# Performance work log

Hardware: AMD Instinct MI355X
Metric: run time of the kernel (lower is better)

Reference implementation:

```python
import jax, jax.numpy as jnp
import numpy as np

B, C_LOW, C_HIGH, KC, VC, H, W = 4, 512, 256, 64, 64, 64, 64


def setup_inputs() -> dict:
    key = jax.random.key(0)
    ks = jax.random.split(key, 6)
    x_low = jax.random.normal(ks[0], (B, C_LOW, H, W), dtype=jnp.float32)
    x_high = jax.random.normal(ks[1], (B, C_HIGH, H, W), dtype=jnp.float32)
    # 1x1 conv weights, fan-in scaled
    Wq = jax.random.normal(ks[2], (KC, C_HIGH), dtype=jnp.float32) / np.sqrt(C_HIGH)
    Wk = jax.random.normal(ks[3], (KC, C_LOW), dtype=jnp.float32) / np.sqrt(C_LOW)
    Wv = jax.random.normal(ks[4], (VC, C_LOW), dtype=jnp.float32) / np.sqrt(C_LOW)
    Wo = jax.random.normal(ks[5], (C_HIGH, VC), dtype=jnp.float32) / np.sqrt(VC)
    return {
        "x_low": x_low, "x_high": x_high,
        "Wq": Wq, "bq": jnp.zeros((KC,), jnp.float32),
        "Wk": Wk, "bk": jnp.zeros((KC,), jnp.float32),
        "Wv": Wv, "bv": jnp.zeros((VC,), jnp.float32),
        "Wo": Wo, "bo": jnp.zeros((C_HIGH,), jnp.float32),
    }


def reference(x_low, x_high, Wq, bq, Wk, bk, Wv, bv, Wo, bo):
    b, ch, h, w = x_high.shape
    n = h * w  # tokens per image
    # 1x1 convs == per-pixel linear maps; flatten spatial to tokens
    xh = x_high.reshape(b, ch, n)                # [B, C_high, N]
    xl = x_low.reshape(b, x_low.shape[1], n)     # [B, C_low,  N]
    q = jnp.einsum('kc,bcn->bnk', Wq, xh) + bq   # [B, N, KC]
    k = jnp.einsum('kc,bcn->bkn', Wk, xl) + bk[:, None]  # [B, KC, N]
    v = jnp.einsum('vc,bcn->bnv', Wv, xl) + bv   # [B, N, VC]
    sim = jnp.einsum('bnk,bkm->bnm', q, k)       # [B, N, N]
    attn = jax.nn.softmax(sim, axis=-1)
    ctx = jnp.einsum('bnm,bmv->bnv', attn, v)    # [B, N, VC]
    out = jnp.einsum('ov,bnv->bon', Wo, ctx) + bo[:, None]  # [B, C_high, N]
    return out.reshape(b, ch, h, w) + x_high
```

## Files before the change

### kernel.cpp

```cpp
#include <hip/hip_runtime.h>
#include <hip/hip_bf16.h>
#include <math.h>
#include <stdint.h>

#define B 4
#define CLOW 512
#define CHIGH 256
#define KC 64
#define VC 64
#define N 4096

typedef __attribute__((ext_vector_type(8))) short bf16x8;
typedef __attribute__((ext_vector_type(4))) short bf16x4;
typedef __attribute__((ext_vector_type(4))) float f32x4;

__device__ inline unsigned short f2bf(float f) {
    union { float f; uint32_t u; } v; v.f = f;
    uint32_t u = v.u;
    u += 0x7fff + ((u >> 16) & 1);
    return (unsigned short)(u >> 16);
}
__device__ inline float bf2f(unsigned short h) {
    union { uint32_t u; float f; } v; v.u = ((uint32_t)h) << 16;
    return v.f;
}
__device__ inline uint32_t packbf2(float a, float b) {
    union { __hip_bfloat16 h; unsigned short u; } ca, cb;
    ca.h = __float2bfloat16(a);
    cb.h = __float2bfloat16(b);
    return (uint32_t)ca.u | ((uint32_t)cb.u << 16);
}
__device__ inline void bfsplit(float x, short* hi, short* lo) {
    union { __hip_bfloat16 h; unsigned short u; } c, d;
    c.h = __float2bfloat16(x);
    d.h = __float2bfloat16(x - __bfloat162float(c.h));
    *hi = (short)c.u; *lo = (short)d.u;
}

#if __has_builtin(__builtin_amdgcn_exp2f)
#define EXP2(x) __builtin_amdgcn_exp2f(x)
#else
#define EXP2(x) exp2f(x)
#endif


#define CSTEP 64
__global__ __launch_bounds__(256) void proj_mfma(
    const float* __restrict__ xl, const float* __restrict__ xh,
    const float* __restrict__ Wq, const float* __restrict__ bq,
    const float* __restrict__ Wk, const float* __restrict__ bk,
    const float* __restrict__ Wv, const float* __restrict__ bv,
    unsigned short* __restrict__ Qt, unsigned short* __restrict__ Kt,
    unsigned short* __restrict__ Vt)
{
    const int proj = blockIdx.z;
    const int b    = blockIdx.y;
    const int bidx = blockIdx.x;
    const int n0   = bidx * 32;
    const int tid  = threadIdx.x;
    const int wv   = tid >> 6;
    const int lane = tid & 63;
    const int lo   = lane & 15;
    const int hi   = lane >> 4;
    const int hi8  = hi * 8;

    __shared__ unsigned short XtHi[32][72];
    __shared__ unsigned short XtLo[32][72];

    const int tS = tid & 3;
    const int t8 = tS * 8;
    const int cR = tid >> 2;

    const float* X; int C;
    if (proj == 0) { X = xh; C = CHIGH; } else { X = xl; C = CLOW; }

    float4 pf0, pf1;

    #define LOADX(C0)                                                            \
        {                                                                        \
            const float* src = X + ((size_t)b*C + (C0) + cR)*N + n0 + t8;        \
            pf0 = *(const float4*)src;                                           \
            pf1 = *(const float4*)(src + 4);                                     \
        }

    #define STAGE()                                                              \
        {                                                                        \
            const int colx = cR ^ (tS << 3);                                     \
            float vv[8] = {pf0.x, pf0.y, pf0.z, pf0.w,                           \
                           pf1.x, pf1.y, pf1.z, pf1.w};                          \
            _Pragma("unroll")                                                    \
            for (int i = 0; i < 8; ++i) {                                        \
                short h_, l_;                                                    \
                bfsplit(vv[i], &h_, &l_);                                        \
                XtHi[t8 + i][colx] = (unsigned short)h_;                         \
                XtLo[t8 + i][colx] = (unsigned short)l_;                         \
            }                                                                    \
        }

    #define WSPLITLD(WP, AH, AL)                                                 \
        {                                                                        \
            float4 w0 = *(const float4*)(WP);                                    \
            float4 w1 = *(const float4*)((WP) + 4);                              \
            float ww[8] = {w0.x,w0.y,w0.z,w0.w,w1.x,w1.y,w1.z,w1.w};             \
            _Pragma("unroll")                                                    \
            for (int i = 0; i < 8; ++i) {                                        \
                short h_, l_;                                                    \
                bfsplit(ww[i], &h_, &l_);                                        \
                AH[i] = h_; AL[i] = l_;                                          \
            }                                                                    \
        }

    const size_t kqFragOff = (size_t)((((wv*2 + (hi>>1)) & 3)*16 + lo)*8 + (hi&1)*4);

    if (proj == 0) {
        f32x4 acc[2];
        #pragma unroll
        for (int t = 0; t < 2; ++t)
            #pragma unroll
            for (int r = 0; r < 4; ++r) acc[t][r] = bq[wv*16 + hi*4 + r];

        LOADX(0)
        for (int c0 = 0; c0 < CHIGH; c0 += CSTEP) {
            STAGE()
            __syncthreads();
            if (c0 + CSTEP < CHIGH) LOADX(c0 + CSTEP)

            #pragma unroll
            for (int m = 0; m < 2; ++m) {
                bf16x8 ah, al;
                const float* wp = Wq + (size_t)(wv*16 + lo)*CHIGH + c0 + m*32 + hi8;
                WSPLITLD(wp, ah, al)
                #pragma unroll
                for (int tt = 0; tt < 2; ++tt) {
                    const int cx = (m*32 + hi8) ^ ((2*tt + (lo >> 3)) << 3);
                    bf16x8 xhv = *(const bf16x8*)&XtHi[tt*16 + lo][cx];
                    bf16x8 xlv = *(const bf16x8*)&XtLo[tt*16 + lo][cx];
                    acc[tt] = __builtin_amdgcn_mfma_f32_16x16x32_bf16(ah, xhv, acc[tt], 0, 0, 0);
                    acc[tt] = __builtin_amdgcn_mfma_f32_16x16x32_bf16(ah, xlv, acc[tt], 0, 0, 0);
                    acc[tt] = __builtin_amdgcn_mfma_f32_16x16x32_bf16(al, xhv, acc[tt], 0, 0, 0);
                }
            }
            __syncthreads();
        }
        const float qs = 1.4426950408889634f;
        #pragma unroll
        for (int t = 0; t < 2; ++t) {
            bf16x4 o;
            #pragma unroll
            for (int r = 0; r < 4; ++r) o[r] = (short)f2bf(acc[t][r] * qs);
            size_t base = (((size_t)b*256 + 2*bidx + t)*2 + (wv>>1))*512;
            *(bf16x4*)&Qt[base + kqFragOff] = o;
        }
    } else {
        f32x4 accK[2], accV[2];
        #pragma unroll
        for (int t = 0; t < 2; ++t)
            #pragma unroll
            for (int r = 0; r < 4; ++r) {
                accK[t][r] = bk[wv*16 + hi*4 + r];
                accV[t][r] = bv[wv*16 + hi*4 + r];
            }

        LOADX(0)
        for (int c0 = 0; c0 < CLOW; c0 += CSTEP) {
            STAGE()
            __syncthreads();
            if (c0 + CSTEP < CLOW) LOADX(c0 + CSTEP)

            #pragma unroll
            for (int m = 0; m < 2; ++m) {
                bf16x8 ahk, alk, ahv, alv;
                const float* wpk = Wk + (size_t)(wv*16 + lo)*CLOW + c0 + m*32 + hi8;
                const float* wpv = Wv + (size_t)(wv*16 + lo)*CLOW + c0 + m*32 + hi8;
                WSPLITLD(wpk, ahk, alk)
                WSPLITLD(wpv, ahv, alv)
                #pragma unroll
                for (int tt = 0; tt < 2; ++tt) {
                    const int cx = (m*32 + hi8) ^ ((2*tt + (lo >> 3)) << 3);
                    bf16x8 xhv = *(const bf16x8*)&XtHi[tt*16 + lo][cx];
                    bf16x8 xlv = *(const bf16x8*)&XtLo[tt*16 + lo][cx];
                    accK[tt] = __builtin_amdgcn_mfma_f32_16x16x32_bf16(ahk, xhv, accK[tt], 0, 0, 0);
                    accK[tt] = __builtin_amdgcn_mfma_f32_16x16x32_bf16(ahk, xlv, accK[tt], 0, 0, 0);
                    accK[tt] = __builtin_amdgcn_mfma_f32_16x16x32_bf16(alk, xhv, accK[tt], 0, 0, 0);
                    accV[tt] = __builtin_amdgcn_mfma_f32_16x16x32_bf16(ahv, xhv, accV[tt], 0, 0, 0);
                    accV[tt] = __builtin_amdgcn_mfma_f32_16x16x32_bf16(ahv, xlv, accV[tt], 0, 0, 0);
                    accV[tt] = __builtin_amdgcn_mfma_f32_16x16x32_bf16(alv, xhv, accV[tt], 0, 0, 0);
                }
            }
            __syncthreads();
        }

        #pragma unroll
        for (int t = 0; t < 2; ++t) {
            bf16x4 o;
            #pragma unroll
            for (int r = 0; r < 4; ++r) o[r] = (short)f2bf(accK[t][r]);
            size_t kbase = (((size_t)b*256 + 2*bidx + t)*2 + (wv>>1))*512;
            *(bf16x4*)&Kt[kbase + kqFragOff] = o;

            const int hi_f = t*2 + (lo >> 3);
            size_t vbase = ((size_t)b*128 + bidx)*2048 + (size_t)wv*512
                         + (size_t)hi_f*128 + (size_t)(lo & 7);
            #pragma unroll
            for (int r = 0; r < 4; ++r)
                Vt[vbase + (size_t)(hi*4 + r)*8] = f2bf(accV[t][r]);
        }
    }
    #undef LOADX
    #undef STAGE
    #undef WSPLITLD
}

#define WSPLIT 8
#define QT 4
__global__ __launch_bounds__(512) void attn(
    const unsigned short* __restrict__ Qt,
    const unsigned short* __restrict__ Kt,
    const unsigned short* __restrict__ Vt,
    float* __restrict__ ctx)
{
    const int bid = blockIdx.x;
    const int xcd = bid & 7;
    const int b   = xcd >> 1;
    const int q0  = ((bid >> 3) * 2 + (xcd & 1)) * 64;

    const int tid  = threadIdx.x;
    const int wv   = tid >> 6;
    const int lane = tid & 63;
    const int lo   = lane & 15;
    const int hi   = lane >> 4;

    __shared__ float Olds[WSPLIT][64][68];
    __shared__ float llds[WSPLIT][64];

    const unsigned short* Kb = Kt + (size_t)b*N*KC;
    const unsigned short* Vb = Vt + (size_t)b*VC*N;
    const unsigned short* Qb = Qt + (size_t)b*N*KC;

    bf16x8 qf[2][QT];
    #pragma unroll
    for (int qt = 0; qt < QT; ++qt) {
        #pragma unroll
        for (int kt = 0; kt < 2; ++kt)
            qf[kt][qt] = *(const bf16x8*)&Qb[(((size_t)(q0>>4) + qt)*2 + kt)*512 + lane*8];
    }

    f32x4 O[4][QT] = {};
    float l_run[QT] = {};

    const int kv0   = wv * (N/WSPLIT);
    const int kvend = kv0 + (N/WSPLIT);

    for (int kv = kv0; kv < kvend; kv += 32) {
        bf16x8 ka[2][2], va[4];
        #pragma unroll
        for (int j = 0; j < 2; ++j)
            #pragma unroll
            for (int m = 0; m < 2; ++m)
                ka[j][m] = *(const bf16x8*)&Kb[(((size_t)(kv>>4) + j)*2 + m)*512 + lane*8];
        #pragma unroll
        for (int vt = 0; vt < 4; ++vt)
            va[vt] = *(const bf16x8*)&Vb[((size_t)(kv>>5))*2048 + vt*512 + lane*8];

        #pragma unroll
        for (int qt = 0; qt < QT; ++qt) {
            f32x4 st[2];
            #pragma unroll
            for (int j = 0; j < 2; ++j) {
                f32x4 z = {};
                z     = __builtin_amdgcn_mfma_f32_16x16x32_bf16(ka[j][0], qf[0][qt], z, 0, 0, 0);
                st[j] = __builtin_amdgcn_mfma_f32_16x16x32_bf16(ka[j][1], qf[1][qt], z, 0, 0, 0);
            }
            uint32_t pk[2][2];
            #pragma unroll
            for (int j = 0; j < 2; ++j) {
                float p0 = EXP2(st[j][0]);
                float p1 = EXP2(st[j][1]);
                float p2 = EXP2(st[j][2]);
                float p3 = EXP2(st[j][3]);
                l_run[qt] += (p0 + p1) + (p2 + p3);
                pk[j][0] = packbf2(p0, p1);
                pk[j][1] = packbf2(p2, p3);
            }
            union { int w[4]; bf16x8 v; } pa;
            #pragma unroll
            for (int w = 0; w < 4; ++w) {
                int src = (2*(hi & 1) + (w >> 1))*16 + lo;
                int t0 = __shfl((int)pk[0][w & 1], src);
                int t1 = __shfl((int)pk[1][w & 1], src);
                pa.w[w] = (hi < 2) ? t0 : t1;
            }
            #pragma unroll
            for (int vt = 0; vt < 4; ++vt)
                O[vt][qt] = __builtin_amdgcn_mfma_f32_16x16x32_bf16(pa.v, va[vt], O[vt][qt], 0, 0, 0);
        }
    }

    #pragma unroll
    for (int qt = 0; qt < QT; ++qt) {
        float s = l_run[qt];
        s += __shfl_xor(s, 16);
        s += __shfl_xor(s, 32);
        l_run[qt] = s;
    }

    #pragma unroll
    for (int qt = 0; qt < QT; ++qt) {
        #pragma unroll
        for (int vt = 0; vt < 4; ++vt)
            #pragma unroll
            for (int r = 0; r < 4; ++r)
                Olds[wv][qt*16 + hi*4 + r][vt*16 + lo] = O[vt][qt][r];
        if (lane < 16) llds[wv][qt*16 + lo] = l_run[qt];
    }
    __syncthreads();

    {
        const int row = tid >> 3;
        const int c8  = (tid & 7) * 8;
        float L = 0.f;
        #pragma unroll
        for (int w = 0; w < WSPLIT; ++w) L += llds[w][row];
        float4 a0 = {0.f,0.f,0.f,0.f}, a1 = {0.f,0.f,0.f,0.f};
        #pragma unroll
        for (int w = 0; w < WSPLIT; ++w) {
            float4 o0 = *(const float4*)&Olds[w][row][c8];
            float4 o1 = *(const float4*)&Olds[w][row][c8 + 4];
            a0.x += o0.x; a0.y += o0.y; a0.z += o0.z; a0.w += o0.w;
            a1.x += o1.x; a1.y += o1.y; a1.z += o1.z; a1.w += o1.w;
        }
        float rL = 1.0f / L;
        a0.x *= rL; a0.y *= rL; a0.z *= rL; a0.w *= rL;
        a1.x *= rL; a1.y *= rL; a1.z *= rL; a1.w *= rL;
        float* cp = &ctx[((size_t)b*N + q0 + row)*VC + c8];
        *(float4*)(cp)     = a0;
        *(float4*)(cp + 4) = a1;
    }
}

__global__ __launch_bounds__(256) void oproj_mfma(
    const float* __restrict__ ctx, const float* __restrict__ Wo,
    const float* __restrict__ bo, const float* __restrict__ xh,
    float* __restrict__ out)
{
    const int b    = blockIdx.y;
    const int n0   = blockIdx.x * 16;
    const int tid  = threadIdx.x;
    const int wv   = tid >> 6;
    const int lane = tid & 63;
    const int lo   = lane & 15;
    const int hi   = lane >> 4;
    const int hi8  = hi * 8;

    bf16x8 bh[2], bl[2];
    const float* cp = ctx + ((size_t)b*N + n0 + lo)*VC + hi8;
    #pragma unroll
    for (int j = 0; j < 2; ++j) {
        float4 c0 = *(const float4*)(cp + j*32);
        float4 c1 = *(const float4*)(cp + j*32 + 4);
        float cc[8] = {c0.x,c0.y,c0.z,c0.w,c1.x,c1.y,c1.z,c1.w};
        #pragma unroll
        for (int i = 0; i < 8; ++i) {
            short h_, l_;
            bfsplit(cc[i], &h_, &l_);
            bh[j][i] = h_;
            bl[j][i] = l_;
        }
    }
    #pragma unroll
    for (int ct = 0; ct < 4; ++ct) {
        const int chan0 = wv*64 + ct*16;
        bf16x8 ah[2], al[2];
        const float* wp = Wo + (size_t)(chan0 + lo)*VC + hi8;
        #pragma unroll
        for (int j = 0; j < 2; ++j) {
            float4 w0 = *(const float4*)(wp + j*32);
            float4 w1 = *(const float4*)(wp + j*32 + 4);
            float ww[8] = {w0.x,w0.y,w0.z,w0.w,w1.x,w1.y,w1.z,w1.w};
            #pragma unroll
            for (int i = 0; i < 8; ++i) {
                short h_, l_;
                bfsplit(ww[i], &h_, &l_);
                ah[j][i] = h_;
                al[j][i] = l_;
            }
        }
        f32x4 acc;
        #pragma unroll
        for (int r = 0; r < 4; ++r) acc[r] = bo[chan0 + hi*4 + r];
        #pragma unroll
        for (int j = 0; j < 2; ++j) {
            acc = __builtin_amdgcn_mfma_f32_16x16x32_bf16(ah[j], bh[j], acc, 0, 0, 0);
            acc = __builtin_amdgcn_mfma_f32_16x16x32_bf16(ah[j], bl[j], acc, 0, 0, 0);
            acc = __builtin_amdgcn_mfma_f32_16x16x32_bf16(al[j], bh[j], acc, 0, 0, 0);
        }
        #pragma unroll
        for (int r = 0; r < 4; ++r) {
            size_t idx = ((size_t)b*CHIGH + chan0 + hi*4 + r)*N + n0 + lo;
            out[idx] = acc[r] + xh[idx];
        }
    }
}

extern "C" void kernel_launch(void* const* d_in, const int* in_sizes, int n_in,
                              void* d_out, int out_size, void* d_ws, size_t ws_size,
                              hipStream_t stream) {
    const float* xl = (const float*)d_in[0];
    const float* xh = (const float*)d_in[1];
    const float* Wq = (const float*)d_in[2];
    const float* bq = (const float*)d_in[3];
    const float* Wk = (const float*)d_in[4];
    const float* bk = (const float*)d_in[5];
    const float* Wv = (const float*)d_in[6];
    const float* bv = (const float*)d_in[7];
    const float* Wo = (const float*)d_in[8];
    const float* bo = (const float*)d_in[9];
    float* out = (float*)d_out;

    unsigned short* Qt = (unsigned short*)d_ws;
    unsigned short* Kt = Qt + (size_t)B*N*KC;
    unsigned short* Vt = Kt + (size_t)B*N*KC;
    float*         ctxp = (float*)(Vt + (size_t)B*VC*N);

    hipLaunchKernelGGL(proj_mfma, dim3(N/32, B, 2), dim3(256), 0, stream,
                       xl, xh, Wq, bq, Wk, bk, Wv, bv, Qt, Kt, Vt);
    hipLaunchKernelGGL(attn, dim3(256), dim3(512), 0, stream,
                       Qt, Kt, Vt, ctxp);
    hipLaunchKernelGGL(oproj_mfma, dim3(N/16, B), dim3(256), 0, stream,
                       ctxp, Wo, bo, xh, out);
}
```

Baseline: 70.22 us.

## Halve projection tile width and double attention KV-split waves per block

```diff
diff --git a/kernel.cpp b/kernel.cpp
--- a/kernel.cpp
+++ b/kernel.cpp
@@ -56,7 +56,7 @@
     const int proj = blockIdx.z;
     const int b    = blockIdx.y;
     const int bidx = blockIdx.x;
-    const int n0   = bidx * 32;
+    const int n0   = bidx * 16;
     const int tid  = threadIdx.x;
     const int wv   = tid >> 6;
     const int lane = tid & 63;
@@ -64,36 +64,32 @@
     const int hi   = lane >> 4;
     const int hi8  = hi * 8;
 
-    __shared__ unsigned short XtHi[32][72];
-    __shared__ unsigned short XtLo[32][72];
-
-    const int tS = tid & 3;
-    const int t8 = tS * 8;
+    __shared__ unsigned short XtHi[16][72];
+    __shared__ unsigned short XtLo[16][72];
+
+    const int t4 = (tid & 3) * 4;
     const int cR = tid >> 2;
 
     const float* X; int C;
     if (proj == 0) { X = xh; C = CHIGH; } else { X = xl; C = CLOW; }
 
-    float4 pf0, pf1;
+    float4 pf0;
 
     #define LOADX(C0)                                                            \
         {                                                                        \
-            const float* src = X + ((size_t)b*C + (C0) + cR)*N + n0 + t8;        \
-            pf0 = *(const float4*)src;                                           \
-            pf1 = *(const float4*)(src + 4);                                     \
+            pf0 = *(const float4*)(X + ((size_t)b*C + (C0) + cR)*N + n0 + t4);   \
         }
 
     #define STAGE()                                                              \
         {                                                                        \
-            const int colx = cR ^ (tS << 3);                                     \
-            float vv[8] = {pf0.x, pf0.y, pf0.z, pf0.w,                           \
-                           pf1.x, pf1.y, pf1.z, pf1.w};                          \
+            const int colx = cR ^ ((tid & 3) << 3);                              \
+            float vv[4] = {pf0.x, pf0.y, pf0.z, pf0.w};                          \
             _Pragma("unroll")                                                    \
-            for (int i = 0; i < 8; ++i) {                                        \
+            for (int i = 0; i < 4; ++i) {                                        \
                 short h_, l_;                                                    \
                 bfsplit(vv[i], &h_, &l_);                                        \
-                XtHi[t8 + i][colx] = (unsigned short)h_;                         \
-                XtLo[t8 + i][colx] = (unsigned short)l_;                         \
+                XtHi[t4 + i][colx] = (unsigned short)h_;                         \
+                XtLo[t4 + i][colx] = (unsigned short)l_;                         \
             }                                                                    \
         }
 
@@ -113,11 +109,9 @@
     const size_t kqFragOff = (size_t)((((wv*2 + (hi>>1)) & 3)*16 + lo)*8 + (hi&1)*4);
 
     if (proj == 0) {
-        f32x4 acc[2];
-        #pragma unroll
-        for (int t = 0; t < 2; ++t)
-            #pragma unroll
-            for (int r = 0; r < 4; ++r) acc[t][r] = bq[wv*16 + hi*4 + r];
+        f32x4 acc;
+        #pragma unroll
+        for (int r = 0; r < 4; ++r) acc[r] = bq[wv*16 + hi*4 + r];
 
         LOADX(0)
         for (int c0 = 0; c0 < CHIGH; c0 += CSTEP) {
@@ -130,36 +124,28 @@
                 bf16x8 ah, al;
                 const float* wp = Wq + (size_t)(wv*16 + lo)*CHIGH + c0 + m*32 + hi8;
                 WSPLITLD(wp, ah, al)
-                #pragma unroll
-                for (int tt = 0; tt < 2; ++tt) {
-                    const int cx = (m*32 + hi8) ^ ((2*tt + (lo >> 3)) << 3);
-                    bf16x8 xhv = *(const bf16x8*)&XtHi[tt*16 + lo][cx];
-                    bf16x8 xlv = *(const bf16x8*)&XtLo[tt*16 + lo][cx];
-                    acc[tt] = __builtin_amdgcn_mfma_f32_16x16x32_bf16(ah, xhv, acc[tt], 0, 0, 0);
-                    acc[tt] = __builtin_amdgcn_mfma_f32_16x16x32_bf16(ah, xlv, acc[tt], 0, 0, 0);
-                    acc[tt] = __builtin_amdgcn_mfma_f32_16x16x32_bf16(al, xhv, acc[tt], 0, 0, 0);
-                }
+                const int cx = (m*32 + hi8) ^ ((lo >> 2) << 3);
+                bf16x8 xhv = *(const bf16x8*)&XtHi[lo][cx];
+                bf16x8 xlv = *(const bf16x8*)&XtLo[lo][cx];
+                acc = __builtin_amdgcn_mfma_f32_16x16x32_bf16(ah, xhv, acc, 0, 0, 0);
+                acc = __builtin_amdgcn_mfma_f32_16x16x32_bf16(ah, xlv, acc, 0, 0, 0);
+                acc = __builtin_amdgcn_mfma_f32_16x16x32_bf16(al, xhv, acc, 0, 0, 0);
             }
             __syncthreads();
         }
         const float qs = 1.4426950408889634f;
-        #pragma unroll
-        for (int t = 0; t < 2; ++t) {
-            bf16x4 o;
-            #pragma unroll
-            for (int r = 0; r < 4; ++r) o[r] = (short)f2bf(acc[t][r] * qs);
-            size_t base = (((size_t)b*256 + 2*bidx + t)*2 + (wv>>1))*512;
-            *(bf16x4*)&Qt[base + kqFragOff] = o;
-        }
+        bf16x4 o;
+        #pragma unroll
+        for (int r = 0; r < 4; ++r) o[r] = (short)f2bf(acc[r] * qs);
+        size_t base = (((size_t)b*256 + bidx)*2 + (wv>>1))*512;
+        *(bf16x4*)&Qt[base + kqFragOff] = o;
     } else {
-        f32x4 accK[2], accV[2];
-        #pragma unroll
-        for (int t = 0; t < 2; ++t)
-            #pragma unroll
-            for (int r = 0; r < 4; ++r) {
-                accK[t][r] = bk[wv*16 + hi*4 + r];
-                accV[t][r] = bv[wv*16 + hi*4 + r];
-            }
+        f32x4 accK, accV;
+        #pragma unroll
+        for (int r = 0; r < 4; ++r) {
+            accK[r] = bk[wv*16 + hi*4 + r];
+            accV[r] = bv[wv*16 + hi*4 + r];
+        }
 
         LOADX(0)
         for (int c0 = 0; c0 < CLOW; c0 += CSTEP) {
@@ -174,46 +160,40 @@
                 const float* wpv = Wv + (size_t)(wv*16 + lo)*CLOW + c0 + m*32 + hi8;
                 WSPLITLD(wpk, ahk, alk)
                 WSPLITLD(wpv, ahv, alv)
-                #pragma unroll
-                for (int tt = 0; tt < 2; ++tt) {
-                    const int cx = (m*32 + hi8) ^ ((2*tt + (lo >> 3)) << 3);
-                    bf16x8 xhv = *(const bf16x8*)&XtHi[tt*16 + lo][cx];
-                    bf16x8 xlv = *(const bf16x8*)&XtLo[tt*16 + lo][cx];
-                    accK[tt] = __builtin_amdgcn_mfma_f32_16x16x32_bf16(ahk, xhv, accK[tt], 0, 0, 0);
-                    accK[tt] = __builtin_amdgcn_mfma_f32_16x16x32_bf16(ahk, xlv, accK[tt], 0, 0, 0);
-                    accK[tt] = __builtin_amdgcn_mfma_f32_16x16x32_bf16(alk, xhv, accK[tt], 0, 0, 0);
-                    accV[tt] = __builtin_amdgcn_mfma_f32_16x16x32_bf16(ahv, xhv, accV[tt], 0, 0, 0);
-                    accV[tt] = __builtin_amdgcn_mfma_f32_16x16x32_bf16(ahv, xlv, accV[tt], 0, 0, 0);
-                    accV[tt] = __builtin_amdgcn_mfma_f32_16x16x32_bf16(alv, xhv, accV[tt], 0, 0, 0);
-                }
+                const int cx = (m*32 + hi8) ^ ((lo >> 2) << 3);
+                bf16x8 xhv = *(const bf16x8*)&XtHi[lo][cx];
+                bf16x8 xlv = *(const bf16x8*)&XtLo[lo][cx];
+                accK = __builtin_amdgcn_mfma_f32_16x16x32_bf16(ahk, xhv, accK, 0, 0, 0);
+                accK = __builtin_amdgcn_mfma_f32_16x16x32_bf16(ahk, xlv, accK, 0, 0, 0);
+                accK = __builtin_amdgcn_mfma_f32_16x16x32_bf16(alk, xhv, accK, 0, 0, 0);
+                accV = __builtin_amdgcn_mfma_f32_16x16x32_bf16(ahv, xhv, accV, 0, 0, 0);
+                accV = __builtin_amdgcn_mfma_f32_16x16x32_bf16(ahv, xlv, accV, 0, 0, 0);
+                accV = __builtin_amdgcn_mfma_f32_16x16x32_bf16(alv, xhv, accV, 0, 0, 0);
             }
             __syncthreads();
         }
 
-        #pragma unroll
-        for (int t = 0; t < 2; ++t) {
-            bf16x4 o;
-            #pragma unroll
-            for (int r = 0; r < 4; ++r) o[r] = (short)f2bf(accK[t][r]);
-            size_t kbase = (((size_t)b*256 + 2*bidx + t)*2 + (wv>>1))*512;
-            *(bf16x4*)&Kt[kbase + kqFragOff] = o;
-
-            const int hi_f = t*2 + (lo >> 3);
-            size_t vbase = ((size_t)b*128 + bidx)*2048 + (size_t)wv*512
-                         + (size_t)hi_f*128 + (size_t)(lo & 7);
-            #pragma unroll
-            for (int r = 0; r < 4; ++r)
-                Vt[vbase + (size_t)(hi*4 + r)*8] = f2bf(accV[t][r]);
-        }
+        bf16x4 o;
+        #pragma unroll
+        for (int r = 0; r < 4; ++r) o[r] = (short)f2bf(accK[r]);
+        size_t kbase = (((size_t)b*256 + bidx)*2 + (wv>>1))*512;
+        *(bf16x4*)&Kt[kbase + kqFragOff] = o;
+
+        const int hi_f = (bidx & 1)*2 + (lo >> 3);
+        size_t vbase = ((size_t)b*128 + (bidx >> 1))*2048 + (size_t)wv*512
+                     + (size_t)hi_f*128 + (size_t)(lo & 7);
+        #pragma unroll
+        for (int r = 0; r < 4; ++r)
+            Vt[vbase + (size_t)(hi*4 + r)*8] = f2bf(accV[r]);
     }
     #undef LOADX
     #undef STAGE
     #undef WSPLITLD
 }
 
-#define WSPLIT 8
+#define WSPLIT 16
 #define QT 4
-__global__ __launch_bounds__(512) void attn(
+__global__ __launch_bounds__(1024, 2) void attn(
     const unsigned short* __restrict__ Qt,
     const unsigned short* __restrict__ Kt,
     const unsigned short* __restrict__ Vt,
@@ -230,7 +210,7 @@
     const int lo   = lane & 15;
     const int hi   = lane >> 4;
 
-    __shared__ float Olds[WSPLIT][64][68];
+    __shared__ float Olds[8][64][68];
     __shared__ float llds[WSPLIT][64];
 
     const unsigned short* Kb = Kt + (size_t)b*N*KC;
@@ -301,40 +281,46 @@
         float s = l_run[qt];
         s += __shfl_xor(s, 16);
         s += __shfl_xor(s, 32);
-        l_run[qt] = s;
-    }
-
-    #pragma unroll
-    for (int qt = 0; qt < QT; ++qt) {
-        #pragma unroll
-        for (int vt = 0; vt < 4; ++vt)
-            #pragma unroll
-            for (int r = 0; r < 4; ++r)
-                Olds[wv][qt*16 + hi*4 + r][vt*16 + lo] = O[vt][qt][r];
-        if (lane < 16) llds[wv][qt*16 + lo] = l_run[qt];
+        if (lane < 16) llds[wv][qt*16 + lo] = s;
+    }
+
+    if (wv >= 8) {
+        #pragma unroll
+        for (int qt = 0; qt < QT; ++qt)
+            #pragma unroll
+            for (int vt = 0; vt < 4; ++vt)
+                #pragma unroll
+                for (int r = 0; r < 4; ++r)
+                    Olds[wv - 8][qt*16 + hi*4 + r][vt*16 + lo] = O[vt][qt][r];
     }
     __syncthreads();
 
+    if (wv < 8) {
+        #pragma unroll
+        for (int qt = 0; qt < QT; ++qt)
+            #pragma unroll
+            for (int vt = 0; vt < 4; ++vt)
+                #pragma unroll
+                for (int r = 0; r < 4; ++r)
+                    Olds[wv][qt*16 + hi*4 + r][vt*16 + lo] += O[vt][qt][r];
+    }
+    __syncthreads();
+
     {
-        const int row = tid >> 3;
-        const int c8  = (tid & 7) * 8;
+        const int row = tid >> 4;
+        const int c4  = (tid & 15) * 4;
         float L = 0.f;
         #pragma unroll
         for (int w = 0; w < WSPLIT; ++w) L += llds[w][row];
-        float4 a0 = {0.f,0.f,0.f,0.f}, a1 = {0.f,0.f,0.f,0.f};
-        #pragma unroll
-        for (int w = 0; w < WSPLIT; ++w) {
-            float4 o0 = *(const float4*)&Olds[w][row][c8];
-            float4 o1 = *(const float4*)&Olds[w][row][c8 + 4];
-            a0.x += o0.x; a0.y += o0.y; a0.z += o0.z; a0.w += o0.w;
-            a1.x += o1.x; a1.y += o1.y; a1.z += o1.z; a1.w += o1.w;
+        float4 o = {0.f, 0.f, 0.f, 0.f};
+        #pragma unroll
+        for (int w = 0; w < 8; ++w) {
+            float4 ow = *(const float4*)&Olds[w][row][c4];
+            o.x += ow.x; o.y += ow.y; o.z += ow.z; o.w += ow.w;
         }
         float rL = 1.0f / L;
-        a0.x *= rL; a0.y *= rL; a0.z *= rL; a0.w *= rL;
-        a1.x *= rL; a1.y *= rL; a1.z *= rL; a1.w *= rL;
-        float* cp = &ctx[((size_t)b*N + q0 + row)*VC + c8];
-        *(float4*)(cp)     = a0;
-        *(float4*)(cp + 4) = a1;
+        o.x *= rL; o.y *= rL; o.z *= rL; o.w *= rL;
+        *(float4*)&ctx[((size_t)b*N + q0 + row)*VC + c4] = o;
     }
 }
 
@@ -422,9 +408,9 @@
     unsigned short* Vt = Kt + (size_t)B*N*KC;
     float*         ctxp = (float*)(Vt + (size_t)B*VC*N);
 
-    hipLaunchKernelGGL(proj_mfma, dim3(N/32, B, 2), dim3(256), 0, stream,
+    hipLaunchKernelGGL(proj_mfma, dim3(N/16, B, 2), dim3(256), 0, stream,
                        xl, xh, Wq, bq, Wk, bk, Wv, bv, Qt, Kt, Vt);
-    hipLaunchKernelGGL(attn, dim3(256), dim3(512), 0, stream,
+    hipLaunchKernelGGL(attn, dim3(256), dim3(1024), 0, stream,
                        Qt, Kt, Vt, ctxp);
     hipLaunchKernelGGL(oproj_mfma, dim3(N/16, B), dim3(256), 0, stream,
                        ctxp, Wo, bo, xh, out);
```

After: 137.9 us. 96.4% more time.

## Split attention KV range across two blocks with atomic partial-sum reduction

Applied to the files above, without the earlier changes.

```diff
diff --git a/kernel.cpp b/kernel.cpp
--- a/kernel.cpp
+++ b/kernel.cpp
@@ -43,6 +43,11 @@
 #define EXP2(x) exp2f(x)
 #endif
 
+
+__global__ __launch_bounds__(256) void zero_ws(float* __restrict__ p) {
+    size_t i = ((size_t)blockIdx.x * 256 + threadIdx.x) * 4;
+    *(float4*)(p + i) = make_float4(0.f, 0.f, 0.f, 0.f);
+}
 
 #define CSTEP 64
 __global__ __launch_bounds__(256) void proj_mfma(
@@ -217,12 +222,13 @@
     const unsigned short* __restrict__ Qt,
     const unsigned short* __restrict__ Kt,
     const unsigned short* __restrict__ Vt,
-    float* __restrict__ ctx)
+    float* __restrict__ ctxsum, float* __restrict__ lsum)
 {
-    const int bid = blockIdx.x;
-    const int xcd = bid & 7;
-    const int b   = xcd >> 1;
-    const int q0  = ((bid >> 3) * 2 + (xcd & 1)) * 64;
+    const int bid  = blockIdx.x;
+    const int xcd  = bid & 7;
+    const int b    = xcd >> 1;
+    const int half = xcd & 1;
+    const int q0   = (bid >> 3) * 64;
 
     const int tid  = threadIdx.x;
     const int wv   = tid >> 6;
@@ -230,7 +236,7 @@
     const int lo   = lane & 15;
     const int hi   = lane >> 4;
 
-    __shared__ float Olds[WSPLIT][64][68];
+    __shared__ float Olds[4][64][68];
     __shared__ float llds[WSPLIT][64];
 
     const unsigned short* Kb = Kt + (size_t)b*N*KC;
@@ -248,8 +254,8 @@
     f32x4 O[4][QT] = {};
     float l_run[QT] = {};
 
-    const int kv0   = wv * (N/WSPLIT);
-    const int kvend = kv0 + (N/WSPLIT);
+    const int kv0   = half*(N/2) + wv * (N/2/WSPLIT);
+    const int kvend = kv0 + (N/2/WSPLIT);
 
     for (int kv = kv0; kv < kvend; kv += 32) {
         bf16x8 ka[2][2], va[4];
@@ -301,17 +307,28 @@
         float s = l_run[qt];
         s += __shfl_xor(s, 16);
         s += __shfl_xor(s, 32);
-        l_run[qt] = s;
-    }
-
-    #pragma unroll
-    for (int qt = 0; qt < QT; ++qt) {
-        #pragma unroll
-        for (int vt = 0; vt < 4; ++vt)
-            #pragma unroll
-            for (int r = 0; r < 4; ++r)
-                Olds[wv][qt*16 + hi*4 + r][vt*16 + lo] = O[vt][qt][r];
-        if (lane < 16) llds[wv][qt*16 + lo] = l_run[qt];
+        if (lane < 16) llds[wv][qt*16 + lo] = s;
+    }
+
+    if (wv >= 4) {
+        #pragma unroll
+        for (int qt = 0; qt < QT; ++qt)
+            #pragma unroll
+            for (int vt = 0; vt < 4; ++vt)
+                #pragma unroll
+                for (int r = 0; r < 4; ++r)
+                    Olds[wv - 4][qt*16 + hi*4 + r][vt*16 + lo] = O[vt][qt][r];
+    }
+    __syncthreads();
+
+    if (wv < 4) {
+        #pragma unroll
+        for (int qt = 0; qt < QT; ++qt)
+            #pragma unroll
+            for (int vt = 0; vt < 4; ++vt)
+                #pragma unroll
+                for (int r = 0; r < 4; ++r)
+                    Olds[wv][qt*16 + hi*4 + r][vt*16 + lo] += O[vt][qt][r];
     }
     __syncthreads();
 
@@ -321,27 +338,25 @@
         float L = 0.f;
         #pragma unroll
         for (int w = 0; w < WSPLIT; ++w) L += llds[w][row];
-        float4 a0 = {0.f,0.f,0.f,0.f}, a1 = {0.f,0.f,0.f,0.f};
-        #pragma unroll
-        for (int w = 0; w < WSPLIT; ++w) {
+        float a[8] = {0.f,0.f,0.f,0.f,0.f,0.f,0.f,0.f};
+        #pragma unroll
+        for (int w = 0; w < 4; ++w) {
             float4 o0 = *(const float4*)&Olds[w][row][c8];
             float4 o1 = *(const float4*)&Olds[w][row][c8 + 4];
-            a0.x += o0.x; a0.y += o0.y; a0.z += o0.z; a0.w += o0.w;
-            a1.x += o1.x; a1.y += o1.y; a1.z += o1.z; a1.w += o1.w;
-        }
-        float rL = 1.0f / L;
-        a0.x *= rL; a0.y *= rL; a0.z *= rL; a0.w *= rL;
-        a1.x *= rL; a1.y *= rL; a1.z *= rL; a1.w *= rL;
-        float* cp = &ctx[((size_t)b*N + q0 + row)*VC + c8];
-        *(float4*)(cp)     = a0;
-        *(float4*)(cp + 4) = a1;
+            a[0] += o0.x; a[1] += o0.y; a[2] += o0.z; a[3] += o0.w;
+            a[4] += o1.x; a[5] += o1.y; a[6] += o1.z; a[7] += o1.w;
+        }
+        float* cp = &ctxsum[((size_t)b*N + q0 + row)*VC + c8];
+        #pragma unroll
+        for (int i = 0; i < 8; ++i) atomicAdd(cp + i, a[i]);
+        if (c8 == 0) atomicAdd(&lsum[(size_t)b*N + q0 + row], L);
     }
 }
 
 __global__ __launch_bounds__(256) void oproj_mfma(
-    const float* __restrict__ ctx, const float* __restrict__ Wo,
-    const float* __restrict__ bo, const float* __restrict__ xh,
-    float* __restrict__ out)
+    const float* __restrict__ ctxsum, const float* __restrict__ lsum,
+    const float* __restrict__ Wo, const float* __restrict__ bo,
+    const float* __restrict__ xh, float* __restrict__ out)
 {
     const int b    = blockIdx.y;
     const int n0   = blockIdx.x * 16;
@@ -352,13 +367,16 @@
     const int hi   = lane >> 4;
     const int hi8  = hi * 8;
 
+    const int n = n0 + lo;
+    const float rL = 1.0f / lsum[(size_t)b*N + n];
     bf16x8 bh[2], bl[2];
-    const float* cp = ctx + ((size_t)b*N + n0 + lo)*VC + hi8;
+    const float* cp = ctxsum + ((size_t)b*N + n)*VC + hi8;
     #pragma unroll
     for (int j = 0; j < 2; ++j) {
         float4 c0 = *(const float4*)(cp + j*32);
         float4 c1 = *(const float4*)(cp + j*32 + 4);
-        float cc[8] = {c0.x,c0.y,c0.z,c0.w,c1.x,c1.y,c1.z,c1.w};
+        float cc[8] = {c0.x*rL, c0.y*rL, c0.z*rL, c0.w*rL,
+                       c1.x*rL, c1.y*rL, c1.z*rL, c1.w*rL};
         #pragma unroll
         for (int i = 0; i < 8; ++i) {
             short h_, l_;
@@ -420,12 +438,14 @@
     unsigned short* Qt = (unsigned short*)d_ws;
     unsigned short* Kt = Qt + (size_t)B*N*KC;
     unsigned short* Vt = Kt + (size_t)B*N*KC;
-    float*         ctxp = (float*)(Vt + (size_t)B*VC*N);
-
+    float*         ctxsum = (float*)(Vt + (size_t)B*VC*N);
+    float*         lsumW  = ctxsum + (size_t)B*N*VC;
+
+    hipLaunchKernelGGL(zero_ws, dim3(1040), dim3(256), 0, stream, ctxsum);
     hipLaunchKernelGGL(proj_mfma, dim3(N/32, B, 2), dim3(256), 0, stream,
                        xl, xh, Wq, bq, Wk, bk, Wv, bv, Qt, Kt, Vt);
-    hipLaunchKernelGGL(attn, dim3(256), dim3(512), 0, stream,
-                       Qt, Kt, Vt, ctxp);
+    hipLaunchKernelGGL(attn, dim3(512), dim3(512), 0, stream,
+                       Qt, Kt, Vt, ctxsum, lsumW);
     hipLaunchKernelGGL(oproj_mfma, dim3(N/16, B), dim3(256), 0, stream,
-                       ctxp, Wo, bo, xh, out);
-}
+                       ctxsum, lsumW, Wo, bo, xh, out);
+}
```

Result: slower. 127.2 us (+81.2%).
